# Performance work log

Hardware: AMD Instinct MI355X
Metric: run time of the kernel (lower is better)

The kernel has to match this reference:

```python
import jax, jax.numpy as jnp
import numpy as np

E = 8  # path_num


def setup_inputs() -> dict:
    key = jax.random.key(0)
    k1, k2, k3 = jax.random.split(key, 3)
    N, D = 8192, 1024
    x = jax.random.normal(k1, (N, D), dtype=jnp.float32)
    hot_mask = jax.random.randint(k2, (N, E), 0, 2, dtype=jnp.int32)  # multi-hot 0/1
    score = jax.random.uniform(k3, (N, E), dtype=jnp.float32)
    return {"x": x, "hot_mask": hot_mask, "score": score}


def reference(x, hot_mask, score):
    # MoE dispatch (route_logic='1d', transform=True):
    # for each expert e, gather tokens n with hot_mask[n, e] == 1 in order,
    # scaled by score[n, e]. Outputs padded to capacity N (zeros beyond count).
    N, D = x.shape
    mask = hot_mask > 0                                   # [N, E]
    ranks = jnp.cumsum(hot_mask, axis=0) - 1              # [N, E] position within expert
    dest = jnp.where(mask, ranks, N)                      # dropped tokens -> dump slot N
    tags = jnp.arange(N, dtype=jnp.int64)                 # flow_tag (arange via pack_invalid_flow)
    scale = score * mask.astype(score.dtype)              # [N, E]

    def per_expert(dest_e, scale_e, mask_e):
        vals = x * scale_e[:, None]                       # [N, D] scaled (zero if not routed)
        out = jnp.zeros((N + 1, D), x.dtype).at[dest_e].add(vals)[:N]
        tag_out = jnp.zeros((N + 1,), jnp.int64).at[dest_e].add(
            jnp.where(mask_e, tags, 0))[:N]               # gathered out_flow_tag, 0-padded
        return out, tag_out

    out_data, out_tags = jax.vmap(per_expert, in_axes=(1, 1, 1))(dest, scale, mask)
    counts = jnp.sum(hot_mask, axis=0)                    # [E] tokens per expert
    return out_data, out_tags, counts
```

## Files before the change

kernel.cpp:

```cpp
#include <hip/hip_runtime.h>

#define N_TOK 8192
#define D_DIM 1024
#define E_NUM 8
#define D4 (D_DIM / 4)
#define SCAN_BLOCKS 32

typedef unsigned long long u64;


__global__ __launch_bounds__(256) void scan_kernel(
    const int4* __restrict__ mask4,
    ulonglong2* __restrict__ prefix,
    ulonglong2* __restrict__ bsum)
{
    const int t = threadIdx.x;
    const int n = blockIdx.x * 256 + t;

    const int4 a = mask4[(size_t)n * 2];
    const int4 b = mask4[(size_t)n * 2 + 1];

    u64 lo = (u64)a.x | ((u64)a.y << 16) | ((u64)a.z << 32) | ((u64)a.w << 48);
    u64 hi = (u64)b.x | ((u64)b.y << 16) | ((u64)b.z << 32) | ((u64)b.w << 48);

    __shared__ u64 slo[256], shi[256];
    slo[t] = lo; shi[t] = hi;
    __syncthreads();

    for (int off = 1; off < 256; off <<= 1) {
        u64 plo = 0, phi = 0;
        if (t >= off) { plo = slo[t - off]; phi = shi[t - off]; }
        __syncthreads();
        if (t >= off) { slo[t] += plo; shi[t] += phi; }
        __syncthreads();
    }

    ulonglong2 ex;
    ex.x = slo[t] - lo;
    ex.y = shi[t] - hi;
    prefix[n] = ex;

    if (t == 255) {
        ulonglong2 tot; tot.x = slo[255]; tot.y = shi[255];
        bsum[blockIdx.x] = tot;
    }
}

__global__ __launch_bounds__(256) void finalize_kernel(
    const int4* __restrict__ mask4,
    const ulonglong2* __restrict__ prefix,
    const ulonglong2* __restrict__ bsum,
    int* __restrict__ dest,
    int* __restrict__ counts_i,
    float* __restrict__ out_tags,
    float* __restrict__ out_counts)
{
    const int bid = blockIdx.x;
    const int t   = threadIdx.x;
    const int n   = bid * 256 + t;

    u64 blo = 0, bhi = 0, tlo = 0, thi = 0;
    #pragma unroll
    for (int k = 0; k < SCAN_BLOCKS; ++k) {
        const ulonglong2 s = bsum[k];
        if (k < bid) { blo += s.x; bhi += s.y; }
        tlo += s.x; thi += s.y;
    }

    const ulonglong2 p = prefix[n];
    const u64 plo = p.x + blo;
    const u64 phi = p.y + bhi;

    const int4 ma = mask4[(size_t)n * 2];
    const int4 mb = mask4[(size_t)n * 2 + 1];
    const int me[8] = { ma.x, ma.y, ma.z, ma.w, mb.x, mb.y, mb.z, mb.w };

    int d[8];
    #pragma unroll
    for (int e = 0; e < E_NUM; ++e) {
        const u64 pk = (e < 4) ? plo : phi;
        const int r  = (int)((pk >> (16 * (e & 3))) & 0xFFFF);
        d[e] = me[e] ? r : -1;
        if (me[e]) out_tags[(size_t)e * N_TOK + r] = (float)n;
    }

    int4* dest4 = (int4*)dest;
    int4 d0; d0.x = d[0]; d0.y = d[1]; d0.z = d[2]; d0.w = d[3];
    int4 d1; d1.x = d[4]; d1.y = d[5]; d1.z = d[6]; d1.w = d[7];
    dest4[(size_t)n * 2]     = d0;
    dest4[(size_t)n * 2 + 1] = d1;

    int cnt[8];
    #pragma unroll
    for (int e = 0; e < E_NUM; ++e) {
        const u64 pk = (e < 4) ? tlo : thi;
        cnt[e] = (int)((pk >> (16 * (e & 3))) & 0xFFFF);
    }

    if (bid == 0 && t < E_NUM) {
        counts_i[t]   = cnt[t];
        out_counts[t] = (float)cnt[t];
    }

    const int g = bid * 256 + t;
    #pragma unroll
    for (int e = 0; e < E_NUM; ++e) {
        for (int idx = cnt[e] + g; idx < N_TOK; idx += N_TOK) {
            out_tags[(size_t)e * N_TOK + idx] = 0.0f;
        }
    }
}

__global__ __launch_bounds__(256) void dispatch_scatter_kernel(
    const float4* __restrict__ x,
    const float* __restrict__ score,
    const int* __restrict__ dest,
    const int* __restrict__ counts_i,
    float4* __restrict__ out)
{
    const int b = blockIdx.x;
    const int c = threadIdx.x;

    if (b < N_TOK) {
        const int n = b;
        const float4 xv = x[(size_t)n * D4 + c];
        #pragma unroll
        for (int e = 0; e < E_NUM; ++e) {
            const int r = dest[(size_t)n * E_NUM + e];
            if (r >= 0) {
                const float s = score[(size_t)n * E_NUM + e];
                float4 v;
                v.x = xv.x * s;
                v.y = xv.y * s;
                v.z = xv.z * s;
                v.w = xv.w * s;
                out[((size_t)e * N_TOK + r) * D4 + c] = v;
            }
        }
    } else {
        const int row = b - N_TOK;
        const int e   = row >> 13;
        const int r   = row & (N_TOK - 1);
        if (r >= counts_i[e]) {
            float4 z;
            z.x = 0.0f; z.y = 0.0f; z.z = 0.0f; z.w = 0.0f;
            out[(size_t)row * D4 + c] = z;
        }
    }
}

extern "C" void kernel_launch(void* const* d_in, const int* in_sizes, int n_in,
                              void* d_out, int out_size, void* d_ws, size_t ws_size,
                              hipStream_t stream) {
    const float* x        = (const float*)d_in[0];
    const int*   hot_mask = (const int*)d_in[1];
    const float* score    = (const float*)d_in[2];

    float* out        = (float*)d_out;
    float* out_data   = out;
    float* out_tags   = out + (size_t)E_NUM * N_TOK * D_DIM;
    float* out_counts = out_tags + (size_t)E_NUM * N_TOK;

    ulonglong2* prefix = (ulonglong2*)d_ws;
    ulonglong2* bsum   = prefix + N_TOK;
    int* dest          = (int*)(bsum + SCAN_BLOCKS);
    int* counts_i      = dest + (size_t)N_TOK * E_NUM;

    scan_kernel<<<SCAN_BLOCKS, 256, 0, stream>>>(
        (const int4*)hot_mask, prefix, bsum);

    finalize_kernel<<<SCAN_BLOCKS, 256, 0, stream>>>(
        (const int4*)hot_mask, prefix, bsum, dest, counts_i, out_tags, out_counts);

    dispatch_scatter_kernel<<<N_TOK + E_NUM * N_TOK, 256, 0, stream>>>(
        (const float4*)x, score, dest, counts_i, (float4*)out_data);
}
```

Measured before the change: 63.53 us.

## Replace scatter dispatch with inverse-map gather writing every output row once

The first pass now only reduces per-block sums, and the finalize kernel does the local scan and builds an inverse source map (token index and score per output slot, -1 for padding). The scatter kernel that wrote routed rows plus a separate zero-fill pass is replaced by a gather kernel that processes 8 output rows per block, reads the source row of x (or emits zeros) and writes with nontemporal stores. This turns scattered writes into sequential contiguous writes and drops the redundant zero-fill branch logic. In exchange x rows are read once per routed expert instead of once per token, which costs extra reads that should mostly hit in cache.

```diff
diff --git a/kernel.cpp b/kernel.cpp
--- a/kernel.cpp
+++ b/kernel.cpp
@@ -5,13 +5,15 @@
 #define E_NUM 8
 #define D4 (D_DIM / 4)
 #define SCAN_BLOCKS 32
+#define ROWS_PER_BLOCK 8
+#define GATHER_BLOCKS (E_NUM * N_TOK / ROWS_PER_BLOCK)
 
 typedef unsigned long long u64;
+typedef float f32x4 __attribute__((ext_vector_type(4)));
 
 
-__global__ __launch_bounds__(256) void scan_kernel(
+__global__ __launch_bounds__(256) void reduce_kernel(
     const int4* __restrict__ mask4,
-    ulonglong2* __restrict__ prefix,
     ulonglong2* __restrict__ bsum)
 {
     const int t = threadIdx.x;
@@ -19,7 +21,6 @@
 
     const int4 a = mask4[(size_t)n * 2];
     const int4 b = mask4[(size_t)n * 2 + 1];
-
     u64 lo = (u64)a.x | ((u64)a.y << 16) | ((u64)a.z << 32) | ((u64)a.w << 48);
     u64 hi = (u64)b.x | ((u64)b.y << 16) | ((u64)b.z << 32) | ((u64)b.w << 48);
 
@@ -27,31 +28,22 @@
     slo[t] = lo; shi[t] = hi;
     __syncthreads();
 
-    for (int off = 1; off < 256; off <<= 1) {
-        u64 plo = 0, phi = 0;
-        if (t >= off) { plo = slo[t - off]; phi = shi[t - off]; }
-        __syncthreads();
-        if (t >= off) { slo[t] += plo; shi[t] += phi; }
+    for (int off = 128; off > 0; off >>= 1) {
+        if (t < off) { slo[t] += slo[t + off]; shi[t] += shi[t + off]; }
         __syncthreads();
     }
 
-    ulonglong2 ex;
-    ex.x = slo[t] - lo;
-    ex.y = shi[t] - hi;
-    prefix[n] = ex;
-
-    if (t == 255) {
-        ulonglong2 tot; tot.x = slo[255]; tot.y = shi[255];
-        bsum[blockIdx.x] = tot;
+    if (t == 0) {
+        ulonglong2 s; s.x = slo[0]; s.y = shi[0];
+        bsum[blockIdx.x] = s;
     }
 }
 
 __global__ __launch_bounds__(256) void finalize_kernel(
     const int4* __restrict__ mask4,
-    const ulonglong2* __restrict__ prefix,
     const ulonglong2* __restrict__ bsum,
-    int* __restrict__ dest,
-    int* __restrict__ counts_i,
+    const float4* __restrict__ score4,
+    int2* __restrict__ srcmap,
     float* __restrict__ out_tags,
     float* __restrict__ out_counts)
 {
@@ -67,28 +59,41 @@
         tlo += s.x; thi += s.y;
     }
 
-    const ulonglong2 p = prefix[n];
-    const u64 plo = p.x + blo;
-    const u64 phi = p.y + bhi;
-
     const int4 ma = mask4[(size_t)n * 2];
     const int4 mb = mask4[(size_t)n * 2 + 1];
-    const int me[8] = { ma.x, ma.y, ma.z, ma.w, mb.x, mb.y, mb.z, mb.w };
+    u64 lo = (u64)ma.x | ((u64)ma.y << 16) | ((u64)ma.z << 32) | ((u64)ma.w << 48);
+    u64 hi = (u64)mb.x | ((u64)mb.y << 16) | ((u64)mb.z << 32) | ((u64)mb.w << 48);
 
-    int d[8];
+    __shared__ u64 slo[256], shi[256];
+    slo[t] = lo; shi[t] = hi;
+    __syncthreads();
+
+    for (int off = 1; off < 256; off <<= 1) {
+        u64 plo = 0, phi = 0;
+        if (t >= off) { plo = slo[t - off]; phi = shi[t - off]; }
+        __syncthreads();
+        if (t >= off) { slo[t] += plo; shi[t] += phi; }
+        __syncthreads();
+    }
+
+    const u64 plo = (slo[t] - lo) + blo;
+    const u64 phi = (shi[t] - hi) + bhi;
+
+    const float4 s0 = score4[(size_t)n * 2];
+    const float4 s1 = score4[(size_t)n * 2 + 1];
+    const int   me[8] = { ma.x, ma.y, ma.z, ma.w, mb.x, mb.y, mb.z, mb.w };
+    const float se[8] = { s0.x, s0.y, s0.z, s0.w, s1.x, s1.y, s1.z, s1.w };
+
     #pragma unroll
     for (int e = 0; e < E_NUM; ++e) {
         const u64 pk = (e < 4) ? plo : phi;
         const int r  = (int)((pk >> (16 * (e & 3))) & 0xFFFF);
-        d[e] = me[e] ? r : -1;
-        if (me[e]) out_tags[(size_t)e * N_TOK + r] = (float)n;
+        if (me[e]) {
+            int2 sm; sm.x = n; sm.y = __float_as_int(se[e]);
+            srcmap[(size_t)e * N_TOK + r]   = sm;
+            out_tags[(size_t)e * N_TOK + r] = (float)n;
+        }
     }
-
-    int4* dest4 = (int4*)dest;
-    int4 d0; d0.x = d[0]; d0.y = d[1]; d0.z = d[2]; d0.w = d[3];
-    int4 d1; d1.x = d[4]; d1.y = d[5]; d1.z = d[6]; d1.w = d[7];
-    dest4[(size_t)n * 2]     = d0;
-    dest4[(size_t)n * 2 + 1] = d1;
 
     int cnt[8];
     #pragma unroll
@@ -97,55 +102,40 @@
         cnt[e] = (int)((pk >> (16 * (e & 3))) & 0xFFFF);
     }
 
-    if (bid == 0 && t < E_NUM) {
-        counts_i[t]   = cnt[t];
-        out_counts[t] = (float)cnt[t];
-    }
+    if (bid == 0 && t < E_NUM) out_counts[t] = (float)cnt[t];
 
-    const int g = bid * 256 + t;
+    const int g = n;
     #pragma unroll
     for (int e = 0; e < E_NUM; ++e) {
-        for (int idx = cnt[e] + g; idx < N_TOK; idx += N_TOK) {
+        const int idx = cnt[e] + g;
+        if (idx < N_TOK) {
+            int2 sm; sm.x = -1; sm.y = 0;
+            srcmap[(size_t)e * N_TOK + idx]   = sm;
             out_tags[(size_t)e * N_TOK + idx] = 0.0f;
         }
     }
 }
 
-__global__ __launch_bounds__(256) void dispatch_scatter_kernel(
-    const float4* __restrict__ x,
-    const float* __restrict__ score,
-    const int* __restrict__ dest,
-    const int* __restrict__ counts_i,
-    float4* __restrict__ out)
+__global__ __launch_bounds__(256) void gather_kernel(
+    const f32x4* __restrict__ x,
+    const int2* __restrict__ srcmap,
+    f32x4* __restrict__ out)
 {
-    const int b = blockIdx.x;
-    const int c = threadIdx.x;
+    const int c    = threadIdx.x;
+    const int row0 = blockIdx.x * ROWS_PER_BLOCK;
 
-    if (b < N_TOK) {
-        const int n = b;
-        const float4 xv = x[(size_t)n * D4 + c];
-        #pragma unroll
-        for (int e = 0; e < E_NUM; ++e) {
-            const int r = dest[(size_t)n * E_NUM + e];
-            if (r >= 0) {
-                const float s = score[(size_t)n * E_NUM + e];
-                float4 v;
-                v.x = xv.x * s;
-                v.y = xv.y * s;
-                v.z = xv.z * s;
-                v.w = xv.w * s;
-                out[((size_t)e * N_TOK + r) * D4 + c] = v;
-            }
+    #pragma unroll
+    for (int i = 0; i < ROWS_PER_BLOCK; ++i) {
+        const int row = row0 + i;
+        const int2 sm = srcmap[row];
+        f32x4 v;
+        if (sm.x >= 0) {
+            const float s = __int_as_float(sm.y);
+            v = x[(size_t)sm.x * D4 + c] * s;
+        } else {
+            v = (f32x4)0.0f;
         }
-    } else {
-        const int row = b - N_TOK;
-        const int e   = row >> 13;
-        const int r   = row & (N_TOK - 1);
-        if (r >= counts_i[e]) {
-            float4 z;
-            z.x = 0.0f; z.y = 0.0f; z.z = 0.0f; z.w = 0.0f;
-            out[(size_t)row * D4 + c] = z;
-        }
+        __builtin_nontemporal_store(v, &out[(size_t)row * D4 + c]);
     }
 }
 
@@ -161,17 +151,16 @@
     float* out_tags   = out + (size_t)E_NUM * N_TOK * D_DIM;
     float* out_counts = out_tags + (size_t)E_NUM * N_TOK;
 
-    ulonglong2* prefix = (ulonglong2*)d_ws;
-    ulonglong2* bsum   = prefix + N_TOK;
-    int* dest          = (int*)(bsum + SCAN_BLOCKS);
-    int* counts_i      = dest + (size_t)N_TOK * E_NUM;
+    ulonglong2* bsum = (ulonglong2*)d_ws;
+    int2* srcmap     = (int2*)(bsum + SCAN_BLOCKS);
 
-    scan_kernel<<<SCAN_BLOCKS, 256, 0, stream>>>(
-        (const int4*)hot_mask, prefix, bsum);
+    reduce_kernel<<<SCAN_BLOCKS, 256, 0, stream>>>(
+        (const int4*)hot_mask, bsum);
 
     finalize_kernel<<<SCAN_BLOCKS, 256, 0, stream>>>(
-        (const int4*)hot_mask, prefix, bsum, dest, counts_i, out_tags, out_counts);
+        (const int4*)hot_mask, bsum, (const float4*)score,
+        srcmap, out_tags, out_counts);
 
-    dispatch_scatter_kernel<<<N_TOK + E_NUM * N_TOK, 256, 0, stream>>>(
-        (const float4*)x, score, dest, counts_i, (float4*)out_data);
+    gather_kernel<<<GATHER_BLOCKS, 256, 0, stream>>>(
+        (const f32x4*)x, srcmap, (f32x4*)out_data);
 }
```

Measured after the change: 70.31 us. +10.7%, slower.

## Fuse scan and finalize into one kernel and use nontemporal output stores

Applied to the files above, without the earlier changes.

Merges the two-pass block scan into a single kernel: each block re-reads the whole mask to compute its own block prefix and the totals redundantly, which removes one launch and the prefix/bsum workspace round-trip. The scatter kernel now writes its large output with nontemporal stores through native vector types, to reduce cache pollution during the heavy write. The cost is redundant mask reads in every block (32x the mask traffic) plus extra shared-memory reductions.

```diff
diff --git a/kernel.cpp b/kernel.cpp
--- a/kernel.cpp
+++ b/kernel.cpp
@@ -7,49 +7,15 @@
 #define SCAN_BLOCKS 32
 
 typedef unsigned long long u64;
+typedef float f32x4 __attribute__((ext_vector_type(4)));
 
 
-__global__ __launch_bounds__(256) void scan_kernel(
-    const int4* __restrict__ mask4,
-    ulonglong2* __restrict__ prefix,
-    ulonglong2* __restrict__ bsum)
-{
-    const int t = threadIdx.x;
-    const int n = blockIdx.x * 256 + t;
-
-    const int4 a = mask4[(size_t)n * 2];
-    const int4 b = mask4[(size_t)n * 2 + 1];
-
-    u64 lo = (u64)a.x | ((u64)a.y << 16) | ((u64)a.z << 32) | ((u64)a.w << 48);
-    u64 hi = (u64)b.x | ((u64)b.y << 16) | ((u64)b.z << 32) | ((u64)b.w << 48);
-
-    __shared__ u64 slo[256], shi[256];
-    slo[t] = lo; shi[t] = hi;
-    __syncthreads();
-
-    for (int off = 1; off < 256; off <<= 1) {
-        u64 plo = 0, phi = 0;
-        if (t >= off) { plo = slo[t - off]; phi = shi[t - off]; }
-        __syncthreads();
-        if (t >= off) { slo[t] += plo; shi[t] += phi; }
-        __syncthreads();
-    }
-
-    ulonglong2 ex;
-    ex.x = slo[t] - lo;
-    ex.y = shi[t] - hi;
-    prefix[n] = ex;
-
-    if (t == 255) {
-        ulonglong2 tot; tot.x = slo[255]; tot.y = shi[255];
-        bsum[blockIdx.x] = tot;
-    }
+__device__ __forceinline__ u64 pack4(const int4 a) {
+    return (u64)a.x | ((u64)a.y << 16) | ((u64)a.z << 32) | ((u64)a.w << 48);
 }
 
-__global__ __launch_bounds__(256) void finalize_kernel(
+__global__ __launch_bounds__(256) void scan_all_kernel(
     const int4* __restrict__ mask4,
-    const ulonglong2* __restrict__ prefix,
-    const ulonglong2* __restrict__ bsum,
     int* __restrict__ dest,
     int* __restrict__ counts_i,
     float* __restrict__ out_tags,
@@ -59,29 +25,53 @@
     const int t   = threadIdx.x;
     const int n   = bid * 256 + t;
 
-    u64 blo = 0, bhi = 0, tlo = 0, thi = 0;
-    #pragma unroll
+    u64 pre_lo = 0, pre_hi = 0, all_lo = 0, all_hi = 0, my_lo = 0, my_hi = 0;
     for (int k = 0; k < SCAN_BLOCKS; ++k) {
-        const ulonglong2 s = bsum[k];
-        if (k < bid) { blo += s.x; bhi += s.y; }
-        tlo += s.x; thi += s.y;
+        const int tok = k * 256 + t;
+        const u64 lo = pack4(mask4[(size_t)tok * 2]);
+        const u64 hi = pack4(mask4[(size_t)tok * 2 + 1]);
+        all_lo += lo; all_hi += hi;
+        if (k < bid)  { pre_lo += lo; pre_hi += hi; }
+        if (k == bid) { my_lo  = lo; my_hi  = hi; }
     }
 
-    const ulonglong2 p = prefix[n];
-    const u64 plo = p.x + blo;
-    const u64 phi = p.y + bhi;
+    __shared__ u64 s1[256], s2[256];
 
-    const int4 ma = mask4[(size_t)n * 2];
-    const int4 mb = mask4[(size_t)n * 2 + 1];
-    const int me[8] = { ma.x, ma.y, ma.z, ma.w, mb.x, mb.y, mb.z, mb.w };
+    s1[t] = all_lo; s2[t] = all_hi; __syncthreads();
+    for (int off = 128; off > 0; off >>= 1) {
+        if (t < off) { s1[t] += s1[t + off]; s2[t] += s2[t + off]; }
+        __syncthreads();
+    }
+    const u64 tot_lo = s1[0], tot_hi = s2[0];
+    __syncthreads();
+
+    s1[t] = pre_lo; s2[t] = pre_hi; __syncthreads();
+    for (int off = 128; off > 0; off >>= 1) {
+        if (t < off) { s1[t] += s1[t + off]; s2[t] += s2[t + off]; }
+        __syncthreads();
+    }
+    const u64 base_lo = s1[0], base_hi = s2[0];
+    __syncthreads();
+
+    s1[t] = my_lo; s2[t] = my_hi; __syncthreads();
+    for (int off = 1; off < 256; off <<= 1) {
+        u64 p1 = 0, p2 = 0;
+        if (t >= off) { p1 = s1[t - off]; p2 = s2[t - off]; }
+        __syncthreads();
+        if (t >= off) { s1[t] += p1; s2[t] += p2; }
+        __syncthreads();
+    }
+    const u64 plo = (s1[t] - my_lo) + base_lo;
+    const u64 phi = (s2[t] - my_hi) + base_hi;
 
     int d[8];
     #pragma unroll
     for (int e = 0; e < E_NUM; ++e) {
-        const u64 pk = (e < 4) ? plo : phi;
-        const int r  = (int)((pk >> (16 * (e & 3))) & 0xFFFF);
-        d[e] = me[e] ? r : -1;
-        if (me[e]) out_tags[(size_t)e * N_TOK + r] = (float)n;
+        const int sh = 16 * (e & 3);
+        const int m  = (int)(((e < 4 ? my_lo : my_hi) >> sh) & 0xFFFF);
+        const int r  = (int)(((e < 4 ? plo   : phi  ) >> sh) & 0xFFFF);
+        d[e] = m ? r : -1;
+        if (m) out_tags[(size_t)e * N_TOK + r] = (float)n;
     }
 
     int4* dest4 = (int4*)dest;
@@ -93,48 +83,40 @@
     int cnt[8];
     #pragma unroll
     for (int e = 0; e < E_NUM; ++e) {
-        const u64 pk = (e < 4) ? tlo : thi;
-        cnt[e] = (int)((pk >> (16 * (e & 3))) & 0xFFFF);
+        cnt[e] = (int)(((e < 4 ? tot_lo : tot_hi) >> (16 * (e & 3))) & 0xFFFF);
     }
-
     if (bid == 0 && t < E_NUM) {
         counts_i[t]   = cnt[t];
         out_counts[t] = (float)cnt[t];
     }
-
-    const int g = bid * 256 + t;
     #pragma unroll
     for (int e = 0; e < E_NUM; ++e) {
-        for (int idx = cnt[e] + g; idx < N_TOK; idx += N_TOK) {
-            out_tags[(size_t)e * N_TOK + idx] = 0.0f;
-        }
+        const int idx = cnt[e] + n;
+        if (idx < N_TOK) out_tags[(size_t)e * N_TOK + idx] = 0.0f;
     }
 }
 
 __global__ __launch_bounds__(256) void dispatch_scatter_kernel(
-    const float4* __restrict__ x,
+    const f32x4* __restrict__ x,
     const float* __restrict__ score,
     const int* __restrict__ dest,
     const int* __restrict__ counts_i,
-    float4* __restrict__ out)
+    f32x4* __restrict__ out)
 {
     const int b = blockIdx.x;
     const int c = threadIdx.x;
 
     if (b < N_TOK) {
         const int n = b;
-        const float4 xv = x[(size_t)n * D4 + c];
+        const f32x4 xv = x[(size_t)n * D4 + c];
         #pragma unroll
         for (int e = 0; e < E_NUM; ++e) {
             const int r = dest[(size_t)n * E_NUM + e];
             if (r >= 0) {
                 const float s = score[(size_t)n * E_NUM + e];
-                float4 v;
-                v.x = xv.x * s;
-                v.y = xv.y * s;
-                v.z = xv.z * s;
-                v.w = xv.w * s;
-                out[((size_t)e * N_TOK + r) * D4 + c] = v;
+                const f32x4 v = xv * s;
+                __builtin_nontemporal_store(
+                    v, &out[((size_t)e * N_TOK + r) * D4 + c]);
             }
         }
     } else {
@@ -142,9 +124,8 @@
         const int e   = row >> 13;
         const int r   = row & (N_TOK - 1);
         if (r >= counts_i[e]) {
-            float4 z;
-            z.x = 0.0f; z.y = 0.0f; z.z = 0.0f; z.w = 0.0f;
-            out[(size_t)row * D4 + c] = z;
+            const f32x4 z = (f32x4)0.0f;
+            __builtin_nontemporal_store(z, &out[(size_t)row * D4 + c]);
         }
     }
 }
@@ -161,17 +142,12 @@
     float* out_tags   = out + (size_t)E_NUM * N_TOK * D_DIM;
     float* out_counts = out_tags + (size_t)E_NUM * N_TOK;
 
-    ulonglong2* prefix = (ulonglong2*)d_ws;
-    ulonglong2* bsum   = prefix + N_TOK;
-    int* dest          = (int*)(bsum + SCAN_BLOCKS);
-    int* counts_i      = dest + (size_t)N_TOK * E_NUM;
+    int* dest     = (int*)d_ws;
+    int* counts_i = dest + (size_t)N_TOK * E_NUM;
 
-    scan_kernel<<<SCAN_BLOCKS, 256, 0, stream>>>(
-        (const int4*)hot_mask, prefix, bsum);
-
-    finalize_kernel<<<SCAN_BLOCKS, 256, 0, stream>>>(
-        (const int4*)hot_mask, prefix, bsum, dest, counts_i, out_tags, out_counts);
+    scan_all_kernel<<<SCAN_BLOCKS, 256, 0, stream>>>(
+        (const int4*)hot_mask, dest, counts_i, out_tags, out_counts);
 
     dispatch_scatter_kernel<<<N_TOK + E_NUM * N_TOK, 256, 0, stream>>>(
-        (const float4*)x, score, dest, counts_i, (float4*)out_data);
+        (const f32x4*)x, score, dest, counts_i, (f32x4*)out_data);
 }
```

After: 60.53 us. -4.7%, faster.
